# Kernel optimization log

Hardware: AMD Instinct MI355X
Metric: run time of the kernel (lower is better)

## Reference

```python
import jax, jax.numpy as jnp
from jax import lax
import numpy as np

MSS = 1448.0
MAX_RTT = 0.01
B, S = 2048, 4096


def setup_inputs() -> dict:
    key = jax.random.key(0)
    k1, k2, k3, k4 = jax.random.split(key, 4)
    # packet lengths in [0, 1500) bytes so bursts aggregate past MSS=1448
    x = jax.random.uniform(k1, (B, S), jnp.float32) * 1500.0
    mask = jax.random.uniform(k2, (B, S)) < 0.1
    scale = 0.00094557476340694
    d_exp = 1e-6 + scale * jax.random.exponential(k3, (B, S), jnp.float32)
    delays = jnp.where(mask, jnp.float32(0.21), d_exp)
    # per-burst RTT samples, indexed by the burst-start packet position
    rtts = jax.random.uniform(k4, (B, S), jnp.float32) * MAX_RTT
    return {"x": x, "delays": delays, "rtts": rtts}


def _simulate_row(x, delays, rtts):
    # x, delays, rtts: [S]
    S_ = x.shape[0]

    def step(carry, inp):
        active, new_burst, r = carry
        xj, dj, rj = inp
        # outer-while check only at burst start: stop forever if x[j] <= 0
        active = jnp.where(new_burst, active & (xj > 0), active)
        r = jnp.where(new_burst, rj, r)
        r_next = r - dj  # inner while: RTT -= delays[j]
        burst_end = active & (r_next <= 0)
        start_flag = new_burst & active
        return (active, burst_end, r_next), (active, start_flag)

    init = (jnp.bool_(True), jnp.bool_(True), jnp.float32(0.0))
    _, (consumed, start_flag) = lax.scan(step, init, (x, delays, rtts))

    # per-burst buffered byte count: segment-sum of consumed packet lengths
    burst_id = jnp.clip(jnp.cumsum(start_flag.astype(jnp.int32)) - 1, 0, S_ - 1)
    buf = jax.ops.segment_sum(jnp.where(consumed, x, 0.0), burst_id, num_segments=S_)

    # `while buf > MSS` emits ceil(buf/MSS)-1 full segments, then remainder
    n_full = jnp.maximum(jnp.ceil(buf / MSS).astype(jnp.int32) - 1, 0)
    rem = buf - n_full.astype(x.dtype) * MSS
    has_rem = rem > 0
    count = n_full + has_rem.astype(jnp.int32)
    starts = jnp.cumsum(count) - count  # exclusive cumsum: output offset per burst
    ends = starts + n_full

    # difference-array trick: positions in [starts, ends) get MSS (OOB drops == truncation)
    diff = (jnp.zeros(S_, jnp.int32)
            .at[starts].add(1, mode='drop')
            .at[ends].add(-1, mode='drop'))
    cover = jnp.cumsum(diff) > 0
    out = jnp.where(cover, jnp.float32(MSS), jnp.float32(0.0))

    # remainder goes right after the MSS run of its burst
    rem_pos = jnp.where(has_rem, ends, S_)  # S_ -> dropped
    out = out.at[rem_pos].set(rem, mode='drop')
    return out


def reference(x, delays, rtts):
    out = jax.vmap(_simulate_row)(x, delays, rtts)  # [B, S]
    return out[..., None]  # unsqueeze(-1) -> [B, S, 1]
```

## Files before the change

### kernel.cpp

```cpp
#include <hip/hip_runtime.h>
#include <math.h>


#define S_LEN 4096
#define BLOCK 512
#define PER   8
#define MSSF  1448.0f

#define OFF_A    0
#define OFF_JA   0
#define OFF_JB   8208
#define OFF_NXT  16416
#define OFF_MRK  24624
#define OFF_WS   26672
#define SMEM_SZ  26704

__device__ __forceinline__ int s2i(int p) { return p ^ (((p >> 6) & 15) << 1); }

__global__ __launch_bounds__(BLOCK, 8) void traffic_kernel(
    const float* __restrict__ gx,
    const float* __restrict__ gd,
    const float* __restrict__ gr,
    float* __restrict__ gout)
{
    __shared__ __align__(16) unsigned char smem[SMEM_SZ];
    float*          s_dly = (float*)(smem + OFF_A);
    unsigned short* s_jA  = (unsigned short*)(smem + OFF_JA);
    unsigned short* s_jB  = (unsigned short*)(smem + OFF_JB);
    float*          s_out = (float*)(smem + OFF_A);
    unsigned short* s_nxt = (unsigned short*)(smem + OFF_NXT);
    unsigned*       s_mrk = (unsigned*)(smem + OFF_MRK);
    int*            s_ws  = (int*)(smem + OFF_WS);

    const int tid = threadIdx.x;
    const size_t rowoff = (size_t)blockIdx.x * S_LEN;
    const float* px = gx + rowoff;
    const float* pd = gd + rowoff;
    const float* pr = gr + rowoff;

    {
        const float4* pd4 = (const float4*)pd;
        float4* s4 = (float4*)s_dly;
        for (int q = tid; q < S_LEN / 4; q += BLOCK) s4[q] = pd4[q];
        if (tid < 8) s_dly[S_LEN + tid] = 1.0e30f;
    }
    float rt[PER];
    unsigned alive = 0;
#pragma unroll
    for (int i = 0; i < PER; ++i) rt[i] = pr[tid + (i << 9)];
#pragma unroll
    for (int i = 0; i < PER; ++i) alive |= (px[tid + (i << 9)] > 0.0f) ? (1u << i) : 0u;
    __syncthreads();

    unsigned surv = 0;
    float rsv[PER];
#pragma unroll
    for (int i = 0; i < PER; ++i) {
        const int p0 = tid + (i << 9);
        const float* dw = s_dly + p0;
        float d0 = dw[0], d1 = dw[1], d2 = dw[2], d3 = dw[3];
        float d4 = dw[4], d5 = dw[5], d6 = dw[6], d7 = dw[7];
        float r1 = rt[i] - d0;
        float r2 = r1 - d1;
        float r3 = r2 - d2;
        float r4 = r3 - d3;
        float r5 = r4 - d4;
        float r6 = r5 - d5;
        float r7 = r6 - d6;
        float r8 = r7 - d7;
        int c = (r1 > 0.0f) + (r2 > 0.0f) + (r3 > 0.0f) + (r4 > 0.0f) +
                (r5 > 0.0f) + (r6 > 0.0f) + (r7 > 0.0f) + (r8 > 0.0f);
        rsv[i] = r8;
        bool al = (alive >> i) & 1u;
        if (al && c == 8) {
            surv |= 1u << i;
        } else {
            int nx = al ? (p0 + c + 1) : S_LEN;
            if (nx > S_LEN) nx = S_LEN;
            s_nxt[s2i(p0)] = (unsigned short)nx;
        }
    }

    while (surv) {
        int i = __ffs(surv) - 1;
        surv &= surv - 1;
        float rr = rsv[0];
#pragma unroll
        for (int ii = 1; ii < PER; ++ii) rr = (i == ii) ? rsv[ii] : rr;
        int p0 = tid + (i << 9);
        int j = p0 + 8;
        int nx;
        while (true) {
            float e0 = s_dly[j],     e1 = s_dly[j + 1];
            float e2 = s_dly[j + 2], e3 = s_dly[j + 3];
            float e4 = s_dly[j + 4], e5 = s_dly[j + 5];
            float e6 = s_dly[j + 6], e7 = s_dly[j + 7];
            float q1 = rr - e0;
            float q2 = q1 - e1;
            float q3 = q2 - e2;
            float q4 = q3 - e3;
            float q5 = q4 - e4;
            float q6 = q5 - e5;
            float q7 = q6 - e6;
            float q8 = q7 - e7;
            int c2 = (q1 > 0.0f) + (q2 > 0.0f) + (q3 > 0.0f) + (q4 > 0.0f) +
                     (q5 > 0.0f) + (q6 > 0.0f) + (q7 > 0.0f) + (q8 > 0.0f);
            if (c2 < 8) { nx = j + c2 + 1; break; }
            j += 8;
            rr = q8;
        }
        if (nx > S_LEN) nx = S_LEN;
        s_nxt[s2i(p0)] = (unsigned short)nx;
    }
    __syncthreads();

    const int sb = tid << 3;
    int own[PER];
    if (tid == 0) { s_jA[4096] = (unsigned short)4096; s_jB[4096] = (unsigned short)4096; }
#pragma unroll
    for (int i = PER - 1; i >= 0; --i) {
        int p = sb + i;
        int v = (int)s_nxt[s2i(p)];
        int e = (v >= sb + PER) ? v : (int)s_jA[s2i(v)];
        s_jA[s2i(p)] = (unsigned short)e;
        own[i] = e;
    }
    s_mrk[tid] = (tid == 0) ? 1u : 0u;
    __syncthreads();

    {
        unsigned short* ja = s_jA;
        unsigned short* jb = s_jB;
        for (int k = 0; k < 9; ++k) {
            unsigned m = s_mrk[tid];
            int q = -1;
            if (m) {
                int p = sb + (__ffs(m) - 1);
                int e = (int)ja[s2i(p)];
                if (e < S_LEN) q = e;
            }
            if (k < 8) {
                int nv[PER];
#pragma unroll
                for (int i = 0; i < PER; ++i) nv[i] = (int)ja[s2i(own[i])];
#pragma unroll
                for (int h = 0; h < PER / 2; ++h) {
                    unsigned w = (unsigned)nv[2 * h] | ((unsigned)nv[2 * h + 1] << 16);
                    *(unsigned*)&jb[s2i(sb + 2 * h)] = w;
                }
#pragma unroll
                for (int i = 0; i < PER; ++i) own[i] = nv[i];
            }
            if (q >= 0) atomicOr(&s_mrk[q >> 3], 1u << (q & 7));
            __syncthreads();
            unsigned short* t = ja; ja = jb; jb = t;
        }
    }

    unsigned lm = 0;
    {
        unsigned m = s_mrk[tid];
        if (m) {
            int p = sb + (__ffs(m) - 1);
            while (p < sb + PER) {
                lm |= 1u << (p - sb);
                p = (int)s_nxt[s2i(p)];
            }
        }
    }

    float bsum[PER];
    unsigned use = 0;
    int tsum = 0;
#pragma unroll
    for (int i = 0; i < PER; ++i) {
        float buf = 0.0f;
        int c = 0;
        if ((lm >> i) & 1u) {
            int p = sb + i;
            int e = (int)s_nxt[s2i(p)];
            float xp = px[p];
            if (xp > 0.0f) {
                use |= 1u << i;
                float sum = xp;
                for (int j = p + 1; j < e; ++j) sum += px[j];
                buf = sum;
                int nf = (int)ceilf(buf / MSSF) - 1; if (nf < 0) nf = 0;
                float rem = buf - (float)nf * MSSF;
                c = nf + (rem > 0.0f ? 1 : 0);
            }
        }
        bsum[i] = buf;
        tsum += c;
    }

    int texcl;
    {
        int lane = tid & 63, wv = tid >> 6;
        int v = tsum;
        for (int off = 1; off < 64; off <<= 1) {
            int u = __shfl_up(v, off, 64);
            if (lane >= off) v += u;
        }
        if (lane == 63) s_ws[wv] = v;
        __syncthreads();
        int woff = 0;
        for (int w = 0; w < wv; ++w) woff += s_ws[w];
        texcl = woff + v - tsum;
    }

    {
        float4* z4 = (float4*)s_out;
        float4 zz; zz.x = zz.y = zz.z = zz.w = 0.0f;
        for (int q = tid; q < S_LEN / 4; q += BLOCK) z4[q] = zz;
    }
    __syncthreads();
    {
        int o = texcl;
#pragma unroll
        for (int i = 0; i < PER; ++i) {
            if ((use >> i) & 1u) {
                float buf = bsum[i];
                int nf = (int)ceilf(buf / MSSF) - 1; if (nf < 0) nf = 0;
                float rem = buf - (float)nf * MSSF;
                int e = o + nf; if (e > S_LEN) e = S_LEN;
                for (int p2 = o; p2 < e; ++p2) s_out[p2] = MSSF;
                int rp = o + nf;
                if (rem > 0.0f && rp < S_LEN) s_out[rp] = rem;
                o += nf + (rem > 0.0f ? 1 : 0);
            }
        }
    }
    __syncthreads();
    {
        float4* po4 = (float4*)(gout + rowoff);
        float4* so4 = (float4*)s_out;
        for (int q = tid; q < S_LEN / 4; q += BLOCK) po4[q] = so4[q];
    }
}

extern "C" void kernel_launch(void* const* d_in, const int* in_sizes, int n_in,
                              void* d_out, int out_size, void* d_ws, size_t ws_size,
                              hipStream_t stream) {
    const float* x      = (const float*)d_in[0];
    const float* delays = (const float*)d_in[1];
    const float* rtts   = (const float*)d_in[2];
    float* out = (float*)d_out;
    int rows = in_sizes[0] / S_LEN;
    traffic_kernel<<<rows, BLOCK, 0, stream>>>(x, delays, rtts, out);
}
```

Baseline: 177.5 us.

## Replace block-compressed pointer jumping with full-array doubling and bitmask marking

Drops the per-thread 8-element chain compression and the serial walk that rebuilt local burst-start masks. Instead it runs plain pointer doubling over all 4096 next-pointers, using strided ownership and an unswizzled jump array. Reachable burst starts are found by having every marked node atomically mark its 2^k-th successor in a 4096-bit shared bitmask. This removes the serial per-thread walk and shrinks the shared-memory footprint, but needs 12 barrier-separated rounds instead of 9 and can issue up to 8 LDS atomics per thread per round.

```diff
diff --git a/kernel.cpp b/kernel.cpp
--- a/kernel.cpp
+++ b/kernel.cpp
@@ -8,12 +8,11 @@
 #define MSSF  1448.0f
 
 #define OFF_A    0
-#define OFF_JA   0
-#define OFF_JB   8208
+#define OFF_JB   8200
 #define OFF_NXT  16416
-#define OFF_MRK  24624
-#define OFF_WS   26672
-#define SMEM_SZ  26704
+#define OFF_MRK  24612
+#define OFF_WS   25124
+#define SMEM_SZ  25160
 
 __device__ __forceinline__ int s2i(int p) { return p ^ (((p >> 6) & 15) << 1); }
 
@@ -25,7 +24,7 @@
 {
     __shared__ __align__(16) unsigned char smem[SMEM_SZ];
     float*          s_dly = (float*)(smem + OFF_A);
-    unsigned short* s_jA  = (unsigned short*)(smem + OFF_JA);
+    unsigned short* s_jA  = (unsigned short*)(smem + OFF_A);
     unsigned short* s_jB  = (unsigned short*)(smem + OFF_JB);
     float*          s_out = (float*)(smem + OFF_A);
     unsigned short* s_nxt = (unsigned short*)(smem + OFF_NXT);
@@ -114,61 +113,46 @@
     }
     __syncthreads();
 
-    const int sb = tid << 3;
     int own[PER];
+#pragma unroll
+    for (int i = 0; i < PER; ++i) {
+        int p = tid + (i << 9);
+        int v = (int)s_nxt[s2i(p)];
+        own[i] = v;
+        s_jA[p] = (unsigned short)v;
+    }
     if (tid == 0) { s_jA[4096] = (unsigned short)4096; s_jB[4096] = (unsigned short)4096; }
-#pragma unroll
-    for (int i = PER - 1; i >= 0; --i) {
-        int p = sb + i;
-        int v = (int)s_nxt[s2i(p)];
-        int e = (v >= sb + PER) ? v : (int)s_jA[s2i(v)];
-        s_jA[s2i(p)] = (unsigned short)e;
-        own[i] = e;
-    }
-    s_mrk[tid] = (tid == 0) ? 1u : 0u;
+    if (tid < 128) s_mrk[tid] = (tid == 0) ? 1u : 0u;
     __syncthreads();
 
     {
         unsigned short* ja = s_jA;
         unsigned short* jb = s_jB;
-        for (int k = 0; k < 9; ++k) {
-            unsigned m = s_mrk[tid];
-            int q = -1;
-            if (m) {
-                int p = sb + (__ffs(m) - 1);
-                int e = (int)ja[s2i(p)];
-                if (e < S_LEN) q = e;
-            }
-            if (k < 8) {
+        for (int k = 0; k < 12; ++k) {
+#pragma unroll
+            for (int i = 0; i < PER; ++i) {
+                unsigned mw = s_mrk[(tid >> 5) + (i << 4)];
+                if ((mw >> (tid & 31)) & 1u) {
+                    int o = own[i];
+                    if (o < S_LEN) atomicOr(&s_mrk[o >> 5], 1u << (o & 31));
+                }
+            }
+            if (k < 11) {
                 int nv[PER];
 #pragma unroll
-                for (int i = 0; i < PER; ++i) nv[i] = (int)ja[s2i(own[i])];
-#pragma unroll
-                for (int h = 0; h < PER / 2; ++h) {
-                    unsigned w = (unsigned)nv[2 * h] | ((unsigned)nv[2 * h + 1] << 16);
-                    *(unsigned*)&jb[s2i(sb + 2 * h)] = w;
-                }
+                for (int i = 0; i < PER; ++i) nv[i] = (int)ja[own[i]];
+#pragma unroll
+                for (int i = 0; i < PER; ++i) jb[tid + (i << 9)] = (unsigned short)nv[i];
 #pragma unroll
                 for (int i = 0; i < PER; ++i) own[i] = nv[i];
             }
-            if (q >= 0) atomicOr(&s_mrk[q >> 3], 1u << (q & 7));
             __syncthreads();
             unsigned short* t = ja; ja = jb; jb = t;
         }
     }
 
-    unsigned lm = 0;
-    {
-        unsigned m = s_mrk[tid];
-        if (m) {
-            int p = sb + (__ffs(m) - 1);
-            while (p < sb + PER) {
-                lm |= 1u << (p - sb);
-                p = (int)s_nxt[s2i(p)];
-            }
-        }
-    }
-
+    const int sb = tid << 3;
+    unsigned mbyte = (s_mrk[tid >> 2] >> ((tid & 3) << 3)) & 0xFFu;
     float bsum[PER];
     unsigned use = 0;
     int tsum = 0;
@@ -176,12 +160,12 @@
     for (int i = 0; i < PER; ++i) {
         float buf = 0.0f;
         int c = 0;
-        if ((lm >> i) & 1u) {
+        if ((mbyte >> i) & 1u) {
             int p = sb + i;
-            int e = (int)s_nxt[s2i(p)];
             float xp = px[p];
             if (xp > 0.0f) {
                 use |= 1u << i;
+                int e = (int)s_nxt[s2i(p)];
                 float sum = xp;
                 for (int j = p + 1; j < e; ++j) sum += px[j];
                 buf = sum;
```

New measurement: 185.6 us. 1.05x slower.

## Replace serial MSS fill loops with difference-array scan and simplify jump tables

Applied to the files above, without the earlier changes.

The per-burst serial loop that wrote MSS into shared memory is replaced by atomic difference-array marks, a block-wide prefix scan and vectorized float4 writes. This is meant to remove load imbalance when a single thread owns a large burst. The pointer-jumping stage drops the swizzled layout, computes local jumps in registers with a single uint4 store, and replaces the atomicOr bitmask of burst starts with a plain store of a per-thread entry index. In exchange the kernel gains extra syncs and a second scan, and it relies on each 8-element chunk being entered at exactly one position.

```diff
diff --git a/kernel.cpp b/kernel.cpp
--- a/kernel.cpp
+++ b/kernel.cpp
@@ -8,12 +8,11 @@
 #define MSSF  1448.0f
 
 #define OFF_A    0
-#define OFF_JA   0
 #define OFF_JB   8208
 #define OFF_NXT  16416
-#define OFF_MRK  24624
-#define OFF_WS   26672
-#define SMEM_SZ  26704
+#define OFF_MENT 24616
+#define OFF_WS   25640
+#define SMEM_SZ  25672
 
 __device__ __forceinline__ int s2i(int p) { return p ^ (((p >> 6) & 15) << 1); }
 
@@ -24,13 +23,14 @@
     float* __restrict__ gout)
 {
     __shared__ __align__(16) unsigned char smem[SMEM_SZ];
-    float*          s_dly = (float*)(smem + OFF_A);
-    unsigned short* s_jA  = (unsigned short*)(smem + OFF_JA);
-    unsigned short* s_jB  = (unsigned short*)(smem + OFF_JB);
-    float*          s_out = (float*)(smem + OFF_A);
-    unsigned short* s_nxt = (unsigned short*)(smem + OFF_NXT);
-    unsigned*       s_mrk = (unsigned*)(smem + OFF_MRK);
-    int*            s_ws  = (int*)(smem + OFF_WS);
+    float*          s_dly  = (float*)(smem + OFF_A);
+    unsigned short* s_jA   = (unsigned short*)(smem + OFF_A);
+    unsigned short* s_jB   = (unsigned short*)(smem + OFF_JB);
+    int*            s_diff = (int*)(smem + OFF_A);
+    float*          s_out  = (float*)(smem + OFF_A);
+    unsigned short* s_nxt  = (unsigned short*)(smem + OFF_NXT);
+    unsigned short* s_ment = (unsigned short*)(smem + OFF_MENT);
+    int*            s_ws   = (int*)(smem + OFF_WS);
 
     const int tid = threadIdx.x;
     const size_t rowoff = (size_t)blockIdx.x * S_LEN;
@@ -115,43 +115,55 @@
     __syncthreads();
 
     const int sb = tid << 3;
-    int own[PER];
+    {
+        int nv[PER], ee[PER];
+#pragma unroll
+        for (int i = 0; i < PER; ++i) nv[i] = (int)s_nxt[s2i(sb + i)];
+#pragma unroll
+        for (int i = PER - 1; i >= 0; --i) {
+            int v = nv[i];
+            int e = v;
+#pragma unroll
+            for (int j2 = i + 1; j2 < PER; ++j2)
+                if (v == sb + j2) e = ee[j2];
+            ee[i] = e;
+        }
+        uint4 pk;
+        pk.x = (unsigned)ee[0] | ((unsigned)ee[1] << 16);
+        pk.y = (unsigned)ee[2] | ((unsigned)ee[3] << 16);
+        pk.z = (unsigned)ee[4] | ((unsigned)ee[5] << 16);
+        pk.w = (unsigned)ee[6] | ((unsigned)ee[7] << 16);
+        *(uint4*)&s_jA[sb] = pk;
+    }
     if (tid == 0) { s_jA[4096] = (unsigned short)4096; s_jB[4096] = (unsigned short)4096; }
-#pragma unroll
-    for (int i = PER - 1; i >= 0; --i) {
-        int p = sb + i;
-        int v = (int)s_nxt[s2i(p)];
-        int e = (v >= sb + PER) ? v : (int)s_jA[s2i(v)];
-        s_jA[s2i(p)] = (unsigned short)e;
-        own[i] = e;
-    }
-    s_mrk[tid] = (tid == 0) ? 1u : 0u;
+    s_ment[tid] = (tid == 0) ? (unsigned short)1 : (unsigned short)0;
     __syncthreads();
 
     {
         unsigned short* ja = s_jA;
         unsigned short* jb = s_jB;
+        int own[PER];
+#pragma unroll
+        for (int i = 0; i < PER; ++i) own[i] = (int)ja[tid + (i << 9)];
         for (int k = 0; k < 9; ++k) {
-            unsigned m = s_mrk[tid];
+            int ent = (int)s_ment[tid];
             int q = -1;
-            if (m) {
-                int p = sb + (__ffs(m) - 1);
-                int e = (int)ja[s2i(p)];
+            if (ent) {
+                int e = (int)ja[ent - 1];
                 if (e < S_LEN) q = e;
             }
             if (k < 8) {
                 int nv[PER];
 #pragma unroll
-                for (int i = 0; i < PER; ++i) nv[i] = (int)ja[s2i(own[i])];
-#pragma unroll
-                for (int h = 0; h < PER / 2; ++h) {
-                    unsigned w = (unsigned)nv[2 * h] | ((unsigned)nv[2 * h + 1] << 16);
-                    *(unsigned*)&jb[s2i(sb + 2 * h)] = w;
-                }
+                for (int i = 0; i < PER; ++i) nv[i] = (int)ja[own[i]];
+                if (q >= 0) s_ment[q >> 3] = (unsigned short)(q + 1);
+#pragma unroll
+                for (int i = 0; i < PER; ++i) jb[tid + (i << 9)] = (unsigned short)nv[i];
 #pragma unroll
                 for (int i = 0; i < PER; ++i) own[i] = nv[i];
-            }
-            if (q >= 0) atomicOr(&s_mrk[q >> 3], 1u << (q & 7));
+            } else {
+                if (q >= 0) s_ment[q >> 3] = (unsigned short)(q + 1);
+            }
             __syncthreads();
             unsigned short* t = ja; ja = jb; jb = t;
         }
@@ -159,9 +171,9 @@
 
     unsigned lm = 0;
     {
-        unsigned m = s_mrk[tid];
-        if (m) {
-            int p = sb + (__ffs(m) - 1);
+        int ent = (int)s_ment[tid];
+        if (ent) {
+            int p = ent - 1;
             while (p < sb + PER) {
                 lm |= 1u << (p - sb);
                 p = (int)s_nxt[s2i(p)];
@@ -178,10 +190,10 @@
         int c = 0;
         if ((lm >> i) & 1u) {
             int p = sb + i;
-            int e = (int)s_nxt[s2i(p)];
             float xp = px[p];
             if (xp > 0.0f) {
                 use |= 1u << i;
+                int e = (int)s_nxt[s2i(p)];
                 float sum = xp;
                 for (int j = p + 1; j < e; ++j) sum += px[j];
                 buf = sum;
@@ -210,11 +222,13 @@
     }
 
     {
-        float4* z4 = (float4*)s_out;
-        float4 zz; zz.x = zz.y = zz.z = zz.w = 0.0f;
-        for (int q = tid; q < S_LEN / 4; q += BLOCK) z4[q] = zz;
-    }
-    __syncthreads();
+        int4* d4 = (int4*)s_diff;
+        int4 z; z.x = z.y = z.z = z.w = 0;
+        d4[tid] = z;
+        d4[tid + 512] = z;
+    }
+    __syncthreads();
+
     {
         int o = texcl;
 #pragma unroll
@@ -223,8 +237,56 @@
                 float buf = bsum[i];
                 int nf = (int)ceilf(buf / MSSF) - 1; if (nf < 0) nf = 0;
                 float rem = buf - (float)nf * MSSF;
-                int e = o + nf; if (e > S_LEN) e = S_LEN;
-                for (int p2 = o; p2 < e; ++p2) s_out[p2] = MSSF;
+                if (nf > 0) {
+                    if (o < S_LEN) atomicAdd(&s_diff[o], 1);
+                    int e2 = o + nf;
+                    if (e2 < S_LEN) atomicAdd(&s_diff[e2], -1);
+                }
+                o += nf + (rem > 0.0f ? 1 : 0);
+            }
+        }
+    }
+    __syncthreads();
+
+    {
+        int4 a = *(int4*)&s_diff[sb];
+        int4 b = *(int4*)&s_diff[sb + 4];
+        int v0 = a.x,      v1 = v0 + a.y, v2 = v1 + a.z, v3 = v2 + a.w;
+        int v4 = v3 + b.x, v5 = v4 + b.y, v6 = v5 + b.z, v7 = v6 + b.w;
+        int T = v7;
+        int lane = tid & 63, wv = tid >> 6;
+        int sc = T;
+        for (int off = 1; off < 64; off <<= 1) {
+            int u = __shfl_up(sc, off, 64);
+            if (lane >= off) sc += u;
+        }
+        if (lane == 63) s_ws[wv] = sc;
+        __syncthreads();
+        int basev = 0;
+        for (int w = 0; w < wv; ++w) basev += s_ws[w];
+        basev += sc - T;
+        float4 fa, fb;
+        fa.x = (basev + v0 > 0) ? MSSF : 0.0f;
+        fa.y = (basev + v1 > 0) ? MSSF : 0.0f;
+        fa.z = (basev + v2 > 0) ? MSSF : 0.0f;
+        fa.w = (basev + v3 > 0) ? MSSF : 0.0f;
+        fb.x = (basev + v4 > 0) ? MSSF : 0.0f;
+        fb.y = (basev + v5 > 0) ? MSSF : 0.0f;
+        fb.z = (basev + v6 > 0) ? MSSF : 0.0f;
+        fb.w = (basev + v7 > 0) ? MSSF : 0.0f;
+        *(float4*)&s_out[sb]     = fa;
+        *(float4*)&s_out[sb + 4] = fb;
+    }
+    __syncthreads();
+
+    {
+        int o = texcl;
+#pragma unroll
+        for (int i = 0; i < PER; ++i) {
+            if ((use >> i) & 1u) {
+                float buf = bsum[i];
+                int nf = (int)ceilf(buf / MSSF) - 1; if (nf < 0) nf = 0;
+                float rem = buf - (float)nf * MSSF;
                 int rp = o + nf;
                 if (rem > 0.0f && rp < S_LEN) s_out[rp] = rem;
                 o += nf + (rem > 0.0f ? 1 : 0);
@@ -232,10 +294,12 @@
         }
     }
     __syncthreads();
+
     {
         float4* po4 = (float4*)(gout + rowoff);
-        float4* so4 = (float4*)s_out;
-        for (int q = tid; q < S_LEN / 4; q += BLOCK) po4[q] = so4[q];
+        const float4* so4 = (const float4*)s_out;
+        po4[tid]       = so4[tid];
+        po4[tid + 512] = so4[tid + 512];
     }
 }
 
```

Result: no change. 174.1 us (-1.9%).
